# Performance work log

Measured on AMD Instinct MI355X. Metric: run time of the kernel, lower is better.

The kernel has to match this reference:

```python
import jax, jax.numpy as jnp
import numpy as np

DELTA = 1e-7
INDEX = (0, 1)  # hops to process, matches init index=[0,1]


def _divide_no_nan(num, den):
    # tf.math.divide_no_nan semantics: 0 where denominator is 0
    safe = jnp.where(den == 0, 1.0, den)
    return jnp.where(den == 0, 0.0, num / safe)


def setup_inputs() -> dict:
    key = jax.random.key(0)
    k1, k2, k3, k4 = jax.random.split(key, 4)
    B, N, F1 = 8, 2048, 4          # F1 = 1 population + 3 SIR features
    T, C = 2, 64                   # hops available, output channels
    input_feature = jax.random.uniform(k1, (B, N, F1), dtype=jnp.float32)
    OD_all = jax.random.uniform(k2, (B, T, N, N), dtype=jnp.float32)
    kernel = jax.random.normal(k3, (3 * 2 ** len(INDEX), C), dtype=jnp.float32)
    bias = jax.random.normal(k4, (C,), dtype=jnp.float32)
    return {"input_feature": input_feature, "OD_all": OD_all,
            "kernel": kernel, "bias": bias}


def reference(input_feature, OD_all, kernel, bias):
    populations = input_feature[:, :, :1]   # [B,N,1]
    SIR = input_feature[:, :, 1:]           # [B,N,F]
    for idx in INDEX:
        OD = OD_all[:, idx]                                  # [B,N,N]
        SIR_n = _divide_no_nan(SIR, DELTA + populations)     # [B,N,F]
        row_sum = jnp.sum(OD, axis=2, keepdims=True)         # [B,N,1]
        ratio = _divide_no_nan(populations, DELTA + row_sum)  # [B,N,1]
        OD = jnp.where(ratio < 1, OD * ratio, OD)            # clip outflow
        OD_out = jnp.sum(OD, axis=2, keepdims=True)          # [B,N,1]
        OD_in = jnp.sum(OD, axis=1)                          # [B,N]
        SIR_in = jnp.einsum('bij,bif->bjf', OD, SIR_n)       # OD^T @ SIR_n
        SIR_stay = SIR - OD_out * SIR_n
        populations = populations - OD_out + OD_in[..., None]
        SIR = jnp.concatenate([SIR_stay, SIR_in], axis=-1)   # doubles F
    output = jnp.einsum('bnf,fc->bnc', SIR, kernel) + bias
    output = jax.nn.relu(output)
    return jnp.concatenate([populations, output], axis=-1)   # [B,N,1+C]
```

## Files before the change

kernel.cpp:

```cpp
#include <hip/hip_runtime.h>


#define DELTA 1e-7f
constexpr int B = 8, N = 2048;
constexpr int NB = B * N;
constexpr int RPB = 64;
constexpr int NRB = N / RPB;

constexpr int ST0_OFF = 0;
constexpr int ST1_OFF = ST0_OFF + NB * 4;
constexpr int P0_OFF  = ST1_OFF + NB * 8;
constexpr int P1_OFF  = P0_OFF + B * NRB * N * 4;

__device__ __forceinline__ void fma4(float4& a, float s, const float4& w) {
  a.x = fmaf(s, w.x, a.x);
  a.y = fmaf(s, w.y, a.y);
  a.z = fmaf(s, w.z, a.z);
  a.w = fmaf(s, w.w, a.w);
}
__device__ __forceinline__ void add4(float4& a, const float4& v) {
  a.x += v.x; a.y += v.y; a.z += v.z; a.w += v.w;
}

__global__ void __launch_bounds__(512) fused0_kernel(const float* __restrict__ OD,
                                                     const float* __restrict__ feat,
                                                     float* __restrict__ part0,
                                                     float* __restrict__ st0) {
  const int tid = threadIdx.x, w = tid >> 6, l = tid & 63;
  const int b = blockIdx.x >> 5, rb = blockIdx.x & 31, i0 = rb * RPB;
  __shared__ float4 ldsfeat[RPB];
  __shared__ float wpart[64];
  __shared__ float4 wv[8];
  if (tid < RPB) ldsfeat[tid] = ((const float4*)feat)[b * N + i0 + tid];
  __syncthreads();

  const float* odbase = OD + ((size_t)(b * 2) * N + i0) * N + w * 256 + l * 4;
  float4 acc[4] = {};
  float4 cur[8], nxt[8];
#pragma unroll
  for (int m = 0; m < 8; ++m) cur[m] = *(const float4*)(odbase + (size_t)m * N);

  for (int g = 0; g < 8; ++g) {
    if (g < 7) {
#pragma unroll
      for (int m = 0; m < 8; ++m)
        nxt[m] = *(const float4*)(odbase + (size_t)((g + 1) * 8 + m) * N);
    }
#pragma unroll
    for (int m = 0; m < 8; ++m) {
      float s = (cur[m].x + cur[m].y) + (cur[m].z + cur[m].w);
#pragma unroll
      for (int off = 32; off; off >>= 1) s += __shfl_down(s, off, 64);
      if (l == 0) wpart[w * 8 + m] = s;
    }
    __syncthreads();
    if (tid < 8) {
      const int r = g * 8 + tid;
      float rs = 0.f;
#pragma unroll
      for (int ww = 0; ww < 8; ++ww) rs += wpart[ww * 8 + tid];
      const float4 f = ldsfeat[r];
      const float pop = f.x;
      const float ratio = pop / (DELTA + rs);
      const float scale = ratio < 1.f ? ratio : 1.f;
      const float inv = 1.f / (DELTA + pop);
      const float odout = scale * rs;
      const float k1 = 1.f - odout * inv;
      ((float4*)st0)[b * N + i0 + r] =
          make_float4(pop - odout, f.y * k1, f.z * k1, f.w * k1);
      wv[tid] = make_float4(scale, scale * f.y * inv, scale * f.z * inv,
                            scale * f.w * inv);
    }
    __syncthreads();
#pragma unroll
    for (int m = 0; m < 8; ++m) {
      const float4 wvm = wv[m];
      fma4(acc[0], cur[m].x, wvm);
      fma4(acc[1], cur[m].y, wvm);
      fma4(acc[2], cur[m].z, wvm);
      fma4(acc[3], cur[m].w, wvm);
    }
    if (g < 7) {
#pragma unroll
      for (int m = 0; m < 8; ++m) cur[m] = nxt[m];
    }
  }
  float4* pb = (float4*)part0 + (size_t)blockIdx.x * N + (w * 256 + l * 4);
#pragma unroll
  for (int c = 0; c < 4; ++c) pb[c] = acc[c];
}

__global__ void __launch_bounds__(512) fused1_kernel(const float* __restrict__ OD,
                                                     const float* __restrict__ st0,
                                                     const float* __restrict__ part0,
                                                     float* __restrict__ part1,
                                                     float* __restrict__ st1) {
  const int tid = threadIdx.x, w = tid >> 6, l = tid & 63;
  const int b = blockIdx.x >> 5, rb = blockIdx.x & 31, i0 = rb * RPB;
  __shared__ float ldspre[RPB * 8];
  __shared__ float4 redp[8][RPB];
  __shared__ float wpart[64];
  __shared__ float4 wva[8], wvb[8];

  {
    const int row = tid & 63, rbg = tid >> 6;
    const float4* p0 = (const float4*)part0 + (size_t)b * NRB * N + i0 + row;
    float4 s = {0.f, 0.f, 0.f, 0.f};
#pragma unroll
    for (int k = 0; k < 4; ++k) add4(s, p0[(size_t)(rbg * 4 + k) * N]);
    redp[rbg][row] = s;
  }
  __syncthreads();
  if (tid < RPB) {
    float4 in = redp[0][tid];
#pragma unroll
    for (int g = 1; g < 8; ++g) add4(in, redp[g][tid]);
    const float4 s0 = ((const float4*)st0)[b * N + i0 + tid];
    const float pop = s0.x + in.x;
    const float inv = 1.f / (DELTA + pop);
    float* o = &ldspre[tid * 8];
    o[0] = pop; o[1] = inv;
    o[2] = s0.y; o[3] = s0.z; o[4] = s0.w;
    o[5] = in.y; o[6] = in.z; o[7] = in.w;
  }
  __syncthreads();

  const float* odbase = OD + ((size_t)(b * 2 + 1) * N + i0) * N + w * 256 + l * 4;
  float4 accA[4] = {}, accB[4] = {};
  float4 cur[8], nxt[8];
#pragma unroll
  for (int m = 0; m < 8; ++m) cur[m] = *(const float4*)(odbase + (size_t)m * N);

  for (int g = 0; g < 8; ++g) {
    if (g < 7) {
#pragma unroll
      for (int m = 0; m < 8; ++m)
        nxt[m] = *(const float4*)(odbase + (size_t)((g + 1) * 8 + m) * N);
    }
#pragma unroll
    for (int m = 0; m < 8; ++m) {
      float s = (cur[m].x + cur[m].y) + (cur[m].z + cur[m].w);
#pragma unroll
      for (int off = 32; off; off >>= 1) s += __shfl_down(s, off, 64);
      if (l == 0) wpart[w * 8 + m] = s;
    }
    __syncthreads();
    if (tid < 8) {
      const int r = g * 8 + tid;
      float rs = 0.f;
#pragma unroll
      for (int ww = 0; ww < 8; ++ww) rs += wpart[ww * 8 + tid];
      const float* pr = &ldspre[r * 8];
      const float pop = pr[0], inv = pr[1];
      const float ratio = pop / (DELTA + rs);
      const float scale = ratio < 1.f ? ratio : 1.f;
      const float odout = scale * rs;
      const float k1 = 1.f - odout * inv;
      float4* s4 = (float4*)st1 + (size_t)(b * N + i0 + r) * 2;
      s4[0] = make_float4(pop - odout, pr[2] * k1, pr[3] * k1, pr[4] * k1);
      s4[1] = make_float4(pr[5] * k1, pr[6] * k1, pr[7] * k1, 0.f);
      const float si = scale * inv;
      wva[tid] = make_float4(scale, pr[2] * si, pr[3] * si, pr[4] * si);
      wvb[tid] = make_float4(pr[5] * si, pr[6] * si, pr[7] * si, 0.f);
    }
    __syncthreads();
#pragma unroll
    for (int m = 0; m < 8; ++m) {
      const float4 wa = wva[m], wb = wvb[m];
      fma4(accA[0], cur[m].x, wa);
      fma4(accB[0], cur[m].x, wb);
      fma4(accA[1], cur[m].y, wa);
      fma4(accB[1], cur[m].y, wb);
      fma4(accA[2], cur[m].z, wa);
      fma4(accB[2], cur[m].z, wb);
      fma4(accA[3], cur[m].w, wa);
      fma4(accB[3], cur[m].w, wb);
    }
    if (g < 7) {
#pragma unroll
      for (int m = 0; m < 8; ++m) cur[m] = nxt[m];
    }
  }
  float4* pb = (float4*)part1 + ((size_t)blockIdx.x * N + (w * 256 + l * 4)) * 2;
#pragma unroll
  for (int c = 0; c < 4; ++c) {
    pb[c * 2] = accA[c];
    pb[c * 2 + 1] = accB[c];
  }
}

__global__ void __launch_bounds__(256) final2_kernel(const float* __restrict__ st1,
                                                     const float* __restrict__ part1,
                                                     const float* __restrict__ kern,
                                                     const float* __restrict__ bias,
                                                     float* __restrict__ out) {
  __shared__ float klds[12 * 64];
  __shared__ float s12[4][16];
  const int tid = threadIdx.x, quad = tid >> 6, c = tid & 63;
  if (tid < 192) ((float4*)klds)[tid] = ((const float4*)kern)[tid];

  const int p = blockIdx.x * 4 + quad;
  const int b = p >> 11, n = p & (N - 1);
  float4 v = ((const float4*)part1)[(((size_t)(b * NRB + (c >> 1)) * N + n) << 1) + (c & 1)];
#pragma unroll
  for (int off = 32; off >= 2; off >>= 1) {
    v.x += __shfl_down(v.x, off, 64);
    v.y += __shfl_down(v.y, off, 64);
    v.z += __shfl_down(v.z, off, 64);
    v.w += __shfl_down(v.w, off, 64);
  }
  if (c == 0) {
    const float4 s0 = ((const float4*)st1)[(size_t)p * 2];
    const float4 s1 = ((const float4*)st1)[(size_t)p * 2 + 1];
    float* o = s12[quad];
    o[0] = s0.y; o[1] = s0.z; o[2] = s0.w;
    o[3] = s1.x; o[4] = s1.y; o[5] = s1.z;
    o[6] = v.y;  o[7] = v.z;  o[8] = v.w;
    o[12] = s0.x + v.x;
  }
  if (c == 1) {
    float* o = s12[quad];
    o[9] = v.x; o[10] = v.y; o[11] = v.z;
  }
  __syncthreads();

  float sum = bias[c];
#pragma unroll
  for (int f = 0; f < 12; ++f) sum += s12[quad][f] * klds[f * 64 + c];
  float* o = out + (size_t)p * 65;
  o[1 + c] = sum > 0.f ? sum : 0.f;
  if (c == 0) o[0] = s12[quad][12];
}

extern "C" void kernel_launch(void* const* d_in, const int* in_sizes, int n_in,
                              void* d_out, int out_size, void* d_ws, size_t ws_size,
                              hipStream_t stream) {
  const float* feat = (const float*)d_in[0];
  const float* OD   = (const float*)d_in[1];
  const float* kern = (const float*)d_in[2];
  const float* bias = (const float*)d_in[3];
  float* out = (float*)d_out;
  float* ws = (float*)d_ws;

  float* st0   = ws + ST0_OFF;
  float* st1   = ws + ST1_OFF;
  float* part0 = ws + P0_OFF;
  float* part1 = ws + P1_OFF;

  fused0_kernel<<<B * NRB, 512, 0, stream>>>(OD, feat, part0, st0);
  fused1_kernel<<<B * NRB, 512, 0, stream>>>(OD, st0, part0, part1, st1);
  final2_kernel<<<NB / 4, 256, 0, stream>>>(st1, part1, kern, bias, out);
}
```

Baseline: 399.3 us.

## Remove per-group barrier by computing row scales redundantly; restructure final reduction kernel

In both fused kernels, every thread now recomputes the per-row scale and weight vectors from double-buffered shared row sums. This removes the second __syncthreads per 8-row group and the serial section where only 8 threads worked. The row-sum shuffle reduction now runs before the next prefetch is issued. The final kernel handles 64 points per 512-thread block, reducing the 32 partial sums with coalesced loads and a register tree instead of cross-lane shuffles. The trade is redundant divides per thread and more registers.

```diff
diff --git a/kernel.cpp b/kernel.cpp
--- a/kernel.cpp
+++ b/kernel.cpp
@@ -6,6 +6,7 @@
 constexpr int NB = B * N;
 constexpr int RPB = 64;
 constexpr int NRB = N / RPB;
+constexpr int PPB = 64;
 
 constexpr int ST0_OFF = 0;
 constexpr int ST1_OFF = ST0_OFF + NB * 4;
@@ -29,9 +30,13 @@
   const int tid = threadIdx.x, w = tid >> 6, l = tid & 63;
   const int b = blockIdx.x >> 5, rb = blockIdx.x & 31, i0 = rb * RPB;
   __shared__ float4 ldsfeat[RPB];
-  __shared__ float wpart[64];
-  __shared__ float4 wv[8];
-  if (tid < RPB) ldsfeat[tid] = ((const float4*)feat)[b * N + i0 + tid];
+  __shared__ float ldsinv[RPB];
+  __shared__ float wpart[2][64];
+  if (tid < RPB) {
+    const float4 f = ((const float4*)feat)[b * N + i0 + tid];
+    ldsfeat[tid] = f;
+    ldsinv[tid] = 1.f / (DELTA + f.x);
+  }
   __syncthreads();
 
   const float* odbase = OD + ((size_t)(b * 2) * N + i0) * N + w * 256 + l * 4;
@@ -41,6 +46,14 @@
   for (int m = 0; m < 8; ++m) cur[m] = *(const float4*)(odbase + (size_t)m * N);
 
   for (int g = 0; g < 8; ++g) {
+#pragma unroll
+    for (int m = 0; m < 8; ++m) {
+      float s = (cur[m].x + cur[m].y) + (cur[m].z + cur[m].w);
+#pragma unroll
+      for (int off = 32; off; off >>= 1) s += __shfl_down(s, off, 64);
+      if (l == 0) wpart[g & 1][w * 8 + m] = s;
+    }
+    __syncthreads();
     if (g < 7) {
 #pragma unroll
       for (int m = 0; m < 8; ++m)
@@ -48,37 +61,26 @@
     }
 #pragma unroll
     for (int m = 0; m < 8; ++m) {
-      float s = (cur[m].x + cur[m].y) + (cur[m].z + cur[m].w);
-#pragma unroll
-      for (int off = 32; off; off >>= 1) s += __shfl_down(s, off, 64);
-      if (l == 0) wpart[w * 8 + m] = s;
-    }
-    __syncthreads();
-    if (tid < 8) {
-      const int r = g * 8 + tid;
+      const int r = g * 8 + m;
       float rs = 0.f;
 #pragma unroll
-      for (int ww = 0; ww < 8; ++ww) rs += wpart[ww * 8 + tid];
+      for (int ww = 0; ww < 8; ++ww) rs += wpart[g & 1][ww * 8 + m];
       const float4 f = ldsfeat[r];
-      const float pop = f.x;
-      const float ratio = pop / (DELTA + rs);
+      const float inv = ldsinv[r];
+      const float ratio = f.x / (DELTA + rs);
       const float scale = ratio < 1.f ? ratio : 1.f;
-      const float inv = 1.f / (DELTA + pop);
-      const float odout = scale * rs;
-      const float k1 = 1.f - odout * inv;
-      ((float4*)st0)[b * N + i0 + r] =
-          make_float4(pop - odout, f.y * k1, f.z * k1, f.w * k1);
-      wv[tid] = make_float4(scale, scale * f.y * inv, scale * f.z * inv,
-                            scale * f.w * inv);
-    }
-    __syncthreads();
-#pragma unroll
-    for (int m = 0; m < 8; ++m) {
-      const float4 wvm = wv[m];
-      fma4(acc[0], cur[m].x, wvm);
-      fma4(acc[1], cur[m].y, wvm);
-      fma4(acc[2], cur[m].z, wvm);
-      fma4(acc[3], cur[m].w, wvm);
+      const float si = scale * inv;
+      const float4 wv = make_float4(scale, f.y * si, f.z * si, f.w * si);
+      fma4(acc[0], cur[m].x, wv);
+      fma4(acc[1], cur[m].y, wv);
+      fma4(acc[2], cur[m].z, wv);
+      fma4(acc[3], cur[m].w, wv);
+      if (tid == m) {
+        const float odout = scale * rs;
+        const float k1 = 1.f - odout * inv;
+        ((float4*)st0)[b * N + i0 + r] =
+            make_float4(f.x - odout, f.y * k1, f.z * k1, f.w * k1);
+      }
     }
     if (g < 7) {
 #pragma unroll
@@ -99,8 +101,7 @@
   const int b = blockIdx.x >> 5, rb = blockIdx.x & 31, i0 = rb * RPB;
   __shared__ float ldspre[RPB * 8];
   __shared__ float4 redp[8][RPB];
-  __shared__ float wpart[64];
-  __shared__ float4 wva[8], wvb[8];
+  __shared__ float wpart[2][64];
 
   {
     const int row = tid & 63, rbg = tid >> 6;
@@ -132,6 +133,14 @@
   for (int m = 0; m < 8; ++m) cur[m] = *(const float4*)(odbase + (size_t)m * N);
 
   for (int g = 0; g < 8; ++g) {
+#pragma unroll
+    for (int m = 0; m < 8; ++m) {
+      float s = (cur[m].x + cur[m].y) + (cur[m].z + cur[m].w);
+#pragma unroll
+      for (int off = 32; off; off >>= 1) s += __shfl_down(s, off, 64);
+      if (l == 0) wpart[g & 1][w * 8 + m] = s;
+    }
+    __syncthreads();
     if (g < 7) {
 #pragma unroll
       for (int m = 0; m < 8; ++m)
@@ -139,34 +148,17 @@
     }
 #pragma unroll
     for (int m = 0; m < 8; ++m) {
-      float s = (cur[m].x + cur[m].y) + (cur[m].z + cur[m].w);
-#pragma unroll
-      for (int off = 32; off; off >>= 1) s += __shfl_down(s, off, 64);
-      if (l == 0) wpart[w * 8 + m] = s;
-    }
-    __syncthreads();
-    if (tid < 8) {
-      const int r = g * 8 + tid;
+      const int r = g * 8 + m;
       float rs = 0.f;
 #pragma unroll
-      for (int ww = 0; ww < 8; ++ww) rs += wpart[ww * 8 + tid];
+      for (int ww = 0; ww < 8; ++ww) rs += wpart[g & 1][ww * 8 + m];
       const float* pr = &ldspre[r * 8];
       const float pop = pr[0], inv = pr[1];
       const float ratio = pop / (DELTA + rs);
       const float scale = ratio < 1.f ? ratio : 1.f;
-      const float odout = scale * rs;
-      const float k1 = 1.f - odout * inv;
-      float4* s4 = (float4*)st1 + (size_t)(b * N + i0 + r) * 2;
-      s4[0] = make_float4(pop - odout, pr[2] * k1, pr[3] * k1, pr[4] * k1);
-      s4[1] = make_float4(pr[5] * k1, pr[6] * k1, pr[7] * k1, 0.f);
       const float si = scale * inv;
-      wva[tid] = make_float4(scale, pr[2] * si, pr[3] * si, pr[4] * si);
-      wvb[tid] = make_float4(pr[5] * si, pr[6] * si, pr[7] * si, 0.f);
-    }
-    __syncthreads();
-#pragma unroll
-    for (int m = 0; m < 8; ++m) {
-      const float4 wa = wva[m], wb = wvb[m];
+      const float4 wa = make_float4(scale, pr[2] * si, pr[3] * si, pr[4] * si);
+      const float4 wb = make_float4(pr[5] * si, pr[6] * si, pr[7] * si, 0.f);
       fma4(accA[0], cur[m].x, wa);
       fma4(accB[0], cur[m].x, wb);
       fma4(accA[1], cur[m].y, wa);
@@ -175,6 +167,13 @@
       fma4(accB[2], cur[m].z, wb);
       fma4(accA[3], cur[m].w, wa);
       fma4(accB[3], cur[m].w, wb);
+      if (tid == m) {
+        const float odout = scale * rs;
+        const float k1 = 1.f - odout * inv;
+        float4* s4 = (float4*)st1 + (size_t)(b * N + i0 + r) * 2;
+        s4[0] = make_float4(pop - odout, pr[2] * k1, pr[3] * k1, pr[4] * k1);
+        s4[1] = make_float4(pr[5] * k1, pr[6] * k1, pr[7] * k1, 0.f);
+      }
     }
     if (g < 7) {
 #pragma unroll
@@ -189,47 +188,51 @@
   }
 }
 
-__global__ void __launch_bounds__(256) final2_kernel(const float* __restrict__ st1,
+__global__ void __launch_bounds__(512) final2_kernel(const float* __restrict__ st1,
                                                      const float* __restrict__ part1,
                                                      const float* __restrict__ kern,
                                                      const float* __restrict__ bias,
                                                      float* __restrict__ out) {
   __shared__ float klds[12 * 64];
-  __shared__ float s12[4][16];
-  const int tid = threadIdx.x, quad = tid >> 6, c = tid & 63;
+  __shared__ float s13[PPB][13];
+  const int tid = threadIdx.x;
+  const int p0 = blockIdx.x * PPB;
+  const int b = p0 >> 11, j0 = p0 & (N - 1);
   if (tid < 192) ((float4*)klds)[tid] = ((const float4*)kern)[tid];
 
-  const int p = blockIdx.x * 4 + quad;
-  const int b = p >> 11, n = p & (N - 1);
-  float4 v = ((const float4*)part1)[(((size_t)(b * NRB + (c >> 1)) * N + n) << 1) + (c & 1)];
-#pragma unroll
-  for (int off = 32; off >= 2; off >>= 1) {
-    v.x += __shfl_down(v.x, off, 64);
-    v.y += __shfl_down(v.y, off, 64);
-    v.z += __shfl_down(v.z, off, 64);
-    v.w += __shfl_down(v.w, off, 64);
-  }
-  if (c == 0) {
-    const float4 s0 = ((const float4*)st1)[(size_t)p * 2];
-    const float4 s1 = ((const float4*)st1)[(size_t)p * 2 + 1];
-    float* o = s12[quad];
-    o[0] = s0.y; o[1] = s0.z; o[2] = s0.w;
-    o[3] = s1.x; o[4] = s1.y; o[5] = s1.z;
-    o[6] = v.y;  o[7] = v.z;  o[8] = v.w;
-    o[12] = s0.x + v.x;
-  }
-  if (c == 1) {
-    float* o = s12[quad];
-    o[9] = v.x; o[10] = v.y; o[11] = v.z;
-  }
-  __syncthreads();
-
-  float sum = bias[c];
-#pragma unroll
-  for (int f = 0; f < 12; ++f) sum += s12[quad][f] * klds[f * 64 + c];
-  float* o = out + (size_t)p * 65;
-  o[1 + c] = sum > 0.f ? sum : 0.f;
-  if (c == 0) o[0] = s12[quad][12];
+  const int j = tid >> 3, f = tid & 7;
+  const float sv = st1[(size_t)p0 * 8 + tid];
+  if (f >= 1 && f <= 6) s13[j][f - 1] = sv;
+
+  const float* pbase = part1 + ((size_t)(b * NRB) * N + j0) * 8 + tid;
+  float v[NRB];
+#pragma unroll
+  for (int r = 0; r < NRB; ++r) v[r] = pbase[(size_t)r * N * 8];
+#pragma unroll
+  for (int s = 1; s < NRB; s <<= 1) {
+#pragma unroll
+    for (int i = 0; i < NRB; i += 2 * s) v[i] += v[i + s];
+  }
+  const float acc = v[0];
+
+  if (f == 0) s13[j][12] = sv + acc;
+  else if (f <= 3) s13[j][5 + f] = acc;
+  else if (f <= 6) s13[j][5 + f] = acc;
+  __syncthreads();
+
+  const int c = tid & 63, pg = tid >> 6;
+  const float bb = bias[c];
+#pragma unroll
+  for (int k = 0; k < 8; ++k) {
+    const int jp = pg * 8 + k;
+    float sum = bb;
+#pragma unroll
+    for (int ff = 0; ff < 12; ++ff)
+      sum += s13[jp][ff] * klds[ff * 64 + c];
+    float* o = out + (size_t)(p0 + jp) * 65;
+    o[1 + c] = sum > 0.f ? sum : 0.f;
+    if (c == 0) o[0] = s13[jp][12];
+  }
 }
 
 extern "C" void kernel_launch(void* const* d_in, const int* in_sizes, int n_in,
@@ -249,5 +252,5 @@
 
   fused0_kernel<<<B * NRB, 512, 0, stream>>>(OD, feat, part0, st0);
   fused1_kernel<<<B * NRB, 512, 0, stream>>>(OD, st0, part0, part1, st1);
-  final2_kernel<<<NB / 4, 256, 0, stream>>>(st1, part1, kern, bias, out);
-}
+  final2_kernel<<<NB / PPB, 512, 0, stream>>>(st1, part1, kern, bias, out);
+}
```

Result: no change. 407.0 us (+1.9%).
